# Optimization experiments

Measured on AMD Instinct MI355X. Metric: run time of the kernel, lower is better.

## Reference

```python
import jax, jax.numpy as jnp
import numpy as np

D_MODEL = 1024
D_INNER = 1024
N_HEADS = 16
HEAD_DIM = D_INNER // N_HEADS  # 64
D_STATE = 16
DT_RANK = 16
CHUNK = 64
PROJ = 2 * D_INNER + 2 * D_STATE * N_HEADS + DT_RANK  # 2576


def setup_inputs() -> dict:
    key = jax.random.key(0)
    ks = jax.random.split(key, 6)
    B, S = 4, 4096
    x = jax.random.normal(ks[0], (B, S, D_MODEL), jnp.float32)
    W_in = jax.random.normal(ks[1], (PROJ, D_MODEL), jnp.float32) * 0.02
    dt_W = jax.random.normal(ks[2], (N_HEADS, DT_RANK), jnp.float32) * 0.1
    dt_b = jax.random.normal(ks[3], (N_HEADS,), jnp.float32) * 0.1
    A_log = jnp.full((N_HEADS,), jnp.log(0.5), jnp.float32)
    D_param = jnp.ones((N_HEADS,), jnp.float32)
    W_out = jax.random.normal(ks[4], (D_MODEL, D_INNER), jnp.float32) * 0.02
    norm_w = jnp.ones((D_INNER,), jnp.float32)
    return dict(x=x, W_in=W_in, dt_W=dt_W, dt_b=dt_b, A_log=A_log,
                D_param=D_param, W_out=W_out, norm_w=norm_w)


def _forward(x, W_in, dt_W, dt_b, A_log, D_param, W_out, norm_w):
    B, S, _ = x.shape
    H, P, N, K = N_HEADS, HEAD_DIM, D_STATE, CHUNK
    proj = x @ W_in.T  # (B,S,PROJ)
    xp = proj[..., :D_INNER]
    z = proj[..., D_INNER:2 * D_INNER]
    o = 2 * D_INNER
    B_ssm = proj[..., o:o + N * H].reshape(B, S, H, N)
    C_ssm = proj[..., o + N * H:o + 2 * N * H].reshape(B, S, H, N)
    dt_low = proj[..., o + 2 * N * H:]
    dt = jax.nn.softplus(dt_low @ dt_W.T + dt_b)  # (B,S,H)
    xp = xp.reshape(B, S, H, P)
    A = -jnp.exp(A_log)  # (H,)

    # --- chunked selective scan (SSD) ---
    nC = S // K  # S chosen divisible by K (original pads otherwise)
    xc = xp.reshape(B, nC, K, H, P)
    dtc = dt.reshape(B, nC, K, H)
    Bc = B_ssm.reshape(B, nC, K, H, N)
    Cc = C_ssm.reshape(B, nC, K, H, N)
    dA = dtc * A  # (B,nC,K,H)
    dAcs = jnp.cumsum(dA, axis=2)
    # intra-chunk quadratic (attention-like) form
    Lm = jnp.exp(dAcs[:, :, :, None, :] - dAcs[:, :, None, :, :])
    causal = jnp.tril(jnp.ones((K, K), jnp.float32))
    Lm = Lm * causal[None, None, :, :, None]
    scores = jnp.einsum('bcihn,bcjhn->bcijh', Cc, Bc) * Lm * dtc[:, :, None, :, :]
    y_intra = jnp.einsum('bcijh,bcjhp->bcihp', scores, xc)
    # per-chunk state contribution
    decay_to_end = jnp.exp(dAcs[:, :, -1:, :] - dAcs)
    wx = (dtc * decay_to_end)[..., None] * xc  # (B,nC,K,H,P)
    chunk_state = jnp.einsum('bckhn,bckhp->bchnp', Bc, wx)  # (B,nC,H,N,P)
    chunk_decay = jnp.exp(dAcs[:, :, -1, :])  # (B,nC,H)

    # cross-chunk recurrence: emit state at chunk START (matches torch loop)
    def step(h, inp):
        d, s = inp
        return d[:, :, None, None] * h + s, h
    h0 = jnp.zeros((B, H, N, P), jnp.float32)
    _, h_states = jax.lax.scan(
        step, h0,
        (jnp.moveaxis(chunk_decay, 1, 0), jnp.moveaxis(chunk_state, 1, 0)))
    h_states = jnp.moveaxis(h_states, 0, 1)  # (B,nC,H,N,P)

    y_cross = jnp.einsum('bcthn,bchnp,bcth->bcthp', Cc, h_states, jnp.exp(dAcs))
    y = (y_intra + y_cross).reshape(B, S, H, P)
    # --- end scan ---

    y = y + xp * D_param[None, None, :, None]
    y = y.reshape(B, S, D_INNER)
    rms = jnp.sqrt(jnp.mean(y * y, axis=-1, keepdims=True) + 1e-6)
    y = y / rms * norm_w
    y = y * jax.nn.silu(z)
    return y @ W_out.T


def reference(x, W_in, dt_W, dt_b, A_log, D_param, W_out, norm_w):
    return _forward(x, W_in, dt_W, dt_b, A_log, D_param, W_out, norm_w)
```

## Files before the change

### kernel.cpp

```cpp
#include <hip/hip_runtime.h>

typedef unsigned short u16;
typedef __attribute__((ext_vector_type(8))) short short8;
typedef __attribute__((ext_vector_type(4))) float f32x4;
typedef __attribute__((ext_vector_type(4))) unsigned short u16x4;
typedef __attribute__((ext_vector_type(8))) unsigned short u16x8;

#define BTOK 16384
#define PROJ_N 2576
#define PROJ_PAD 2816
#define DK 1024
#define NCH 256
#define NH 16
#define HD 64
#define NS 16

__device__ __forceinline__ float b2f(u16 b) {
    union { unsigned int u; float f; } v; v.u = ((unsigned int)b) << 16; return v.f;
}
__device__ __forceinline__ u16 f2b(float f) {
    union { float f; unsigned int u; } v; v.f = f;
    unsigned int r = v.u + 0x7fffu + ((v.u >> 16) & 1u);
    return (u16)(r >> 16);
}

__device__ __forceinline__ void stage_asm(const u16* g, const u16* l) {
    unsigned loff = (unsigned)(size_t)(const __attribute__((address_space(3))) u16*)l;
    unsigned su = __builtin_amdgcn_readfirstlane(loff);
    asm volatile("s_mov_b32 m0, %1\n\t"
                 "global_load_lds_dwordx4 %0, off"
                 :: "v"(g), "s"(su));
}

template <int IMM>
__device__ __forceinline__ short8 dsr128(unsigned a) {
    short8 d;
    asm volatile("ds_read_b128 %0, %1 offset:%2" : "=v"(d) : "v"(a), "i"(IMM));
    return d;
}

#define LGKM(n) do { asm volatile("s_waitcnt lgkmcnt(" #n ")"); __builtin_amdgcn_sched_barrier(0); } while (0)
#define MFMA_B16 __builtin_amdgcn_mfma_f32_16x16x32_bf16

__global__ __launch_bounds__(256) void cast_bf16(const float* __restrict__ s,
                                                 u16* __restrict__ d, int n4) {
    int t = blockIdx.x * 256 + threadIdx.x;
    if (t < n4) {
        float4 v = ((const float4*)s)[t];
        u16x4 o; o.x = f2b(v.x); o.y = f2b(v.y); o.z = f2b(v.z); o.w = f2b(v.w);
        ((u16x4*)d)[t] = o;
    }
}

__global__ __launch_bounds__(256) void cast_pad_win(const float* __restrict__ s,
                                                    u16* __restrict__ d) {
    int t = blockIdx.x * 256 + threadIdx.x;
    int i4 = t * 4;
    float4 v = make_float4(0.f, 0.f, 0.f, 0.f);
    if (i4 < PROJ_N * DK) v = ((const float4*)s)[t];
    u16x4 o; o.x = f2b(v.x); o.y = f2b(v.y); o.z = f2b(v.z); o.w = f2b(v.w);
    ((u16x4*)d)[t] = o;
}

#define MT 64

template <int OUT_BF16>
__global__ __launch_bounds__(512, 2) void gemm8(const u16* __restrict__ A,
                                                const u16* __restrict__ B,
                                                float* __restrict__ Cf,
                                                u16* __restrict__ Cb,
                                                int K, int ldc) {
    extern __shared__ u16 smem[];
    u16* AsU = smem;
    const int tid = threadIdx.x;
    const int wave = tid >> 6, lane = tid & 63;
    const int wr = wave >> 2, wc = wave & 3;
    const int m_l = lane & 15, quad = lane >> 4;

    const int b = blockIdx.x;
    const int bm = (b & 7) * 8 + ((b >> 3) & 7);
    const int bn = b >> 6;

    const u16* Ab = A + (long)bm * 256 * K;
    const u16* Bb = B + (long)bn * 256 * K;

    const unsigned lds0 = (unsigned)(size_t)(const __attribute__((address_space(3))) u16*)smem;
    const int sw = m_l & 7;
    const unsigned a0b = lds0 + (wr * 128 + m_l) * 128 + (quad ^ sw) * 16;
    const unsigned a1b = lds0 + (wr * 128 + m_l) * 128 + ((4 + quad) ^ sw) * 16;
    const unsigned b0b = lds0 + 65536 + (wc * 64 + m_l) * 128 + (quad ^ sw) * 16;
    const unsigned b1b = lds0 + 65536 + (wc * 64 + m_l) * 128 + ((4 + quad) ^ sw) * 16;

    const int srow = tid >> 3;
    const int schk = (tid & 7) ^ (srow & 7);
    const int sdst = wave * 512;

    f32x4 acc[8][4];
#pragma unroll
    for (int f = 0; f < 8; ++f)
#pragma unroll
        for (int n = 0; n < 4; ++n) acc[f][n] = (f32x4){0.f, 0.f, 0.f, 0.f};

    const int NT = K >> 6;

    auto stage = [&](const u16* G, u16* L, int q, int k0) {
        stage_asm(G + (long)(q * 64 + srow) * K + k0 + schk * 8,
                  L + q * 4096 + sdst);
    };
    u16* BsU = smem + 32768;

    stage(Ab, AsU, 0, 0); stage(Ab, AsU, 2, 0);
    stage(Bb, BsU, 0, 0); stage(Bb, BsU, 1, 0); stage(Bb, BsU, 2, 0); stage(Bb, BsU, 3, 0);
    stage(Ab, AsU, 1, 0); stage(Ab, AsU, 3, 0);
    stage(Ab, AsU + 16384, 0, 64); stage(Ab, AsU + 16384, 2, 64);
    asm volatile("s_waitcnt vmcnt(2)");
    __builtin_amdgcn_s_barrier();

    short8 af[4][2], bf[4][2];
    af[0][0] = dsr128<0>(a0b);    af[0][1] = dsr128<0>(a1b);
    af[1][0] = dsr128<2048>(a0b); af[1][1] = dsr128<2048>(a1b);
    af[2][0] = dsr128<4096>(a0b); af[2][1] = dsr128<4096>(a1b);
    af[3][0] = dsr128<6144>(a0b); af[3][1] = dsr128<6144>(a1b);
    bf[0][0] = dsr128<0>(b0b);    bf[0][1] = dsr128<0>(b1b);
    bf[1][0] = dsr128<2048>(b0b); bf[1][1] = dsr128<2048>(b1b);

    int cur = 0;
    for (int t = 0; t < NT; ++t) {
        const unsigned cB = ((unsigned)cur) << 15;
        const unsigned a0 = a0b + cB, a1 = a1b + cB, b0 = b0b + cB, b1 = b1b + cB;
        const int cbu = cur << 14;
        u16* Anxt = AsU + (cbu ^ 16384);
        u16* Bnxt = BsU + (cbu ^ 16384);
        u16* Acur = AsU + cbu;
        const int k1 = (t + 1) << 6, k2 = (t + 2) << 6;
        const bool s1 = (t + 1 < NT), s2 = (t + 2 < NT);

        bf[2][0] = dsr128<4096>(b0); bf[2][1] = dsr128<4096>(b1);
        bf[3][0] = dsr128<6144>(b0); bf[3][1] = dsr128<6144>(b1);
        if (s1) { stage(Bb, Bnxt, 0, k1); stage(Bb, Bnxt, 1, k1);
                  stage(Bb, Bnxt, 2, k1); stage(Bb, Bnxt, 3, k1); }
        __builtin_amdgcn_s_barrier();
        LGKM(4);
        __builtin_amdgcn_s_setprio(1);
#pragma unroll
        for (int f = 0; f < 4; ++f)
#pragma unroll
            for (int n = 0; n < 2; ++n) {
                acc[f][n] = MFMA_B16(af[f][0], bf[n][0], acc[f][n], 0, 0, 0);
                acc[f][n] = MFMA_B16(af[f][1], bf[n][1], acc[f][n], 0, 0, 0);
            }
        __builtin_amdgcn_s_setprio(0);
        __builtin_amdgcn_sched_barrier(0);

        LGKM(0);
        __builtin_amdgcn_s_setprio(1);
#pragma unroll
        for (int f = 0; f < 4; ++f)
#pragma unroll
            for (int n = 0; n < 2; ++n) {
                acc[f][2 + n] = MFMA_B16(af[f][0], bf[2 + n][0], acc[f][2 + n], 0, 0, 0);
                acc[f][2 + n] = MFMA_B16(af[f][1], bf[2 + n][1], acc[f][2 + n], 0, 0, 0);
            }
        __builtin_amdgcn_s_setprio(0);
        __builtin_amdgcn_sched_barrier(0);
        if (s1) { stage(Ab, Anxt, 1, k1); stage(Ab, Anxt, 3, k1); }
        if (s1) { asm volatile("s_waitcnt vmcnt(8)"); }
        else    { asm volatile("s_waitcnt vmcnt(0)"); }
        __builtin_amdgcn_s_barrier();

        af[0][0] = dsr128<8192>(a0);  af[0][1] = dsr128<8192>(a1);
        af[1][0] = dsr128<10240>(a0); af[1][1] = dsr128<10240>(a1);
        af[2][0] = dsr128<12288>(a0); af[2][1] = dsr128<12288>(a1);
        af[3][0] = dsr128<14336>(a0); af[3][1] = dsr128<14336>(a1);
        if (s2) { stage(Ab, Acur, 0, k2); stage(Ab, Acur, 2, k2); }
        __builtin_amdgcn_s_setprio(1);
        LGKM(6);
#pragma unroll
        for (int n = 0; n < 2; ++n) {
            acc[4][n] = MFMA_B16(af[0][0], bf[n][0], acc[4][n], 0, 0, 0);
            acc[4][n] = MFMA_B16(af[0][1], bf[n][1], acc[4][n], 0, 0, 0);
        }
        LGKM(4);
#pragma unroll
        for (int n = 0; n < 2; ++n) {
            acc[5][n] = MFMA_B16(af[1][0], bf[n][0], acc[5][n], 0, 0, 0);
            acc[5][n] = MFMA_B16(af[1][1], bf[n][1], acc[5][n], 0, 0, 0);
        }
        LGKM(2);
#pragma unroll
        for (int n = 0; n < 2; ++n) {
            acc[6][n] = MFMA_B16(af[2][0], bf[n][0], acc[6][n], 0, 0, 0);
            acc[6][n] = MFMA_B16(af[2][1], bf[n][1], acc[6][n], 0, 0, 0);
        }
        LGKM(0);
#pragma unroll
        for (int n = 0; n < 2; ++n) {
            acc[7][n] = MFMA_B16(af[3][0], bf[n][0], acc[7][n], 0, 0, 0);
            acc[7][n] = MFMA_B16(af[3][1], bf[n][1], acc[7][n], 0, 0, 0);
        }
#pragma unroll
        for (int f = 0; f < 4; ++f)
#pragma unroll
            for (int n = 0; n < 2; ++n) {
                acc[4 + f][2 + n] = MFMA_B16(af[f][0], bf[2 + n][0], acc[4 + f][2 + n], 0, 0, 0);
                acc[4 + f][2 + n] = MFMA_B16(af[f][1], bf[2 + n][1], acc[4 + f][2 + n], 0, 0, 0);
            }
        __builtin_amdgcn_s_setprio(0);
        __builtin_amdgcn_sched_barrier(0);

        if (s1 && s2)      { asm volatile("s_waitcnt vmcnt(4)"); }
        else if (s1)       { asm volatile("s_waitcnt vmcnt(2)"); }
        __builtin_amdgcn_s_barrier();
        if (s1) {
            const unsigned nB = cB ^ 32768u;
            const unsigned na0 = a0b + nB, na1 = a1b + nB, nb0 = b0b + nB, nb1 = b1b + nB;
            af[0][0] = dsr128<0>(na0);    af[0][1] = dsr128<0>(na1);
            af[1][0] = dsr128<2048>(na0); af[1][1] = dsr128<2048>(na1);
            af[2][0] = dsr128<4096>(na0); af[2][1] = dsr128<4096>(na1);
            af[3][0] = dsr128<6144>(na0); af[3][1] = dsr128<6144>(na1);
            bf[0][0] = dsr128<0>(nb0);    bf[0][1] = dsr128<0>(nb1);
            bf[1][0] = dsr128<2048>(nb0); bf[1][1] = dsr128<2048>(nb1);
        }
        cur ^= 1;
    }

#pragma unroll
    for (int f = 0; f < 8; ++f) {
        int row_base = bm * 256 + wr * 128 + f * 16 + quad * 4;
#pragma unroll
        for (int n = 0; n < 4; ++n) {
            int col = bn * 256 + wc * 64 + n * 16 + m_l;
#pragma unroll
            for (int r = 0; r < 4; ++r) {
                float v = acc[f][n][r];
                long off = (long)(row_base + r) * ldc + col;
                if (OUT_BF16) Cb[off] = f2b(v);
                else          Cf[off] = v;
            }
        }
    }
}

__global__ __launch_bounds__(256) void ssm_intra(const u16* __restrict__ proj,
                                                 const float* __restrict__ dt_W,
                                                 const float* __restrict__ dt_b,
                                                 const float* __restrict__ A_log,
                                                 float* __restrict__ dAcs,
                                                 float* __restrict__ decay,
                                                 u16* __restrict__ y_acc,
                                                 float* __restrict__ cstate) {
    int bch = blockIdx.x;
    int bc = bch >> 4, h = bch & 15;
    long tok0 = (long)bc * 64;
    __shared__ float Cs[64][20], Bm[64][20];
    __shared__ u16 Sh[64][72], Sl[64][72];
    __shared__ u16 Xt[64][72];
    __shared__ u16 Wh[64][72], Wl[64][72];
    __shared__ u16 Bt[16][72];
    __shared__ float dts[64], dAs[64], wk[64];
    const int tid = threadIdx.x;
    const int wave = tid >> 6, lane = tid & 63;
    const int m_l = lane & 15, quad = lane >> 4;

    if (tid < 64) {
        long tok = tok0 + tid;
        u16x8 lo0 = *(const u16x8*)&proj[tok * PROJ_PAD + 2560];
        u16x8 lo1 = *(const u16x8*)&proj[tok * PROJ_PAD + 2568];
        float a = dt_b[h];
#pragma unroll
        for (int r = 0; r < 8; ++r) a += b2f(lo0[r]) * dt_W[h * 16 + r];
#pragma unroll
        for (int r = 0; r < 8; ++r) a += b2f(lo1[r]) * dt_W[h * 16 + 8 + r];
        float d = (a > 20.f) ? a : log1pf(__expf(a));
        float dA = -__expf(A_log[h]) * d;
        float cs = dA;
#pragma unroll
        for (int off = 1; off < 64; off <<= 1) {
            float o = __shfl_up(cs, off, 64);
            if (tid >= off) cs += o;
        }
        float cs63 = __shfl(cs, 63, 64);
        dts[tid] = d;
        dAs[tid] = cs;
        wk[tid] = d * __expf(cs63 - cs);
        dAcs[tok * 16 + h] = cs;
        if (tid == 63) decay[bc * 16 + h] = __expf(cs);
    }
#pragma unroll
    for (int it = 0; it < 4; ++it) {
        int li = it * 256 + tid;
        int i = li >> 4, n = li & 15;
        u16 cb = proj[(tok0 + i) * PROJ_PAD + 2304 + h * 16 + n];
        u16 bb = proj[(tok0 + i) * PROJ_PAD + 2048 + h * 16 + n];
        Cs[i][n] = b2f(cb);
        Bm[i][n] = b2f(bb);
        Bt[n][i] = bb;
    }
    __syncthreads();
#pragma unroll
    for (int it = 0; it < 2; ++it) {
        int li = it * 256 + tid;
        int j = li & 63, p0 = (li >> 6) * 8;
        u16x8 xv = *(const u16x8*)&proj[(tok0 + j) * PROJ_PAD + h * 64 + p0];
        float w = wk[j];
#pragma unroll
        for (int t = 0; t < 8; ++t) {
            u16 xb = xv[t];
            Xt[p0 + t][j] = xb;
            float v = w * b2f(xb);
            u16 hi = f2b(v);
            Wh[p0 + t][j] = hi;
            Wl[p0 + t][j] = f2b(v - b2f(hi));
        }
    }
    {
        int j = tid & 63, i0 = tid >> 6;
#pragma unroll
        for (int g = 0; g < 16; ++g) {
            int i = i0 + g * 4;
            float v = 0.f;
            if (j <= i) {
                float d = 0.f;
                const f32x4* cp = (const f32x4*)Cs[i];
                const f32x4* bp = (const f32x4*)Bm[j];
#pragma unroll
                for (int n4 = 0; n4 < 4; ++n4) {
                    f32x4 c = cp[n4], b = bp[n4];
                    d += c.x * b.x + c.y * b.y + c.z * b.z + c.w * b.w;
                }
                v = d * __expf(dAs[i] - dAs[j]) * dts[j];
            }
            u16 hi = f2b(v);
            Sh[i][j] = hi;
            Sl[i][j] = f2b(v - b2f(hi));
        }
    }
    __syncthreads();
    {
        f32x4 yv[4];
#pragma unroll
        for (int jt = 0; jt < 4; ++jt) yv[jt] = (f32x4){0.f, 0.f, 0.f, 0.f};
#pragma unroll
        for (int ks = 0; ks < 2; ++ks) {
            int kc = ks * 32 + quad * 8;
            short8 ah = *(const short8*)&Sh[wave * 16 + m_l][kc];
            short8 al = *(const short8*)&Sl[wave * 16 + m_l][kc];
#pragma unroll
            for (int jt = 0; jt < 4; ++jt) {
                short8 bx = *(const short8*)&Xt[jt * 16 + m_l][kc];
                yv[jt] = MFMA_B16(ah, bx, yv[jt], 0, 0, 0);
                yv[jt] = MFMA_B16(al, bx, yv[jt], 0, 0, 0);
            }
        }
#pragma unroll
        for (int jt = 0; jt < 4; ++jt)
#pragma unroll
            for (int r = 0; r < 4; ++r) {
                int i = wave * 16 + quad * 4 + r;
                int p = jt * 16 + m_l;
                y_acc[(tok0 + i) * 1024 + h * 64 + p] = f2b(yv[jt][r]);
            }
    }
    {
        f32x4 cacc = (f32x4){0.f, 0.f, 0.f, 0.f};
#pragma unroll
        for (int ks = 0; ks < 2; ++ks) {
            int kc = ks * 32 + quad * 8;
            short8 a = *(const short8*)&Bt[m_l][kc];
            short8 bh = *(const short8*)&Wh[wave * 16 + m_l][kc];
            short8 bl = *(const short8*)&Wl[wave * 16 + m_l][kc];
            cacc = MFMA_B16(a, bh, cacc, 0, 0, 0);
            cacc = MFMA_B16(a, bl, cacc, 0, 0, 0);
        }
#pragma unroll
        for (int r = 0; r < 4; ++r) {
            int n = quad * 4 + r;
            int p = wave * 16 + m_l;
            cstate[(long)bch * 1024 + n * 64 + p] = cacc[r];
        }
    }
}

__global__ __launch_bounds__(256) void scan_chunks(const float* __restrict__ cs,
                                                   const float* __restrict__ decay,
                                                   float* __restrict__ hs) {
    int t = blockIdx.x * 256 + threadIdx.x;
    int p = t & 63, n = (t >> 6) & 15, h = (t >> 10) & 15, b = t >> 14;
    float state = 0.f;
    for (int c = 0; c < 64; ++c) {
        long idx = (((long)((b * 64 + c) * 16 + h)) * 16 + n) * 64 + p;
        hs[idx] = state;
        state = decay[(b * 64 + c) * 16 + h] * state + cs[idx];
    }
}

__global__ __launch_bounds__(256) void ssm_cross(const u16* __restrict__ proj,
                                                 const float* __restrict__ dAcs,
                                                 const float* __restrict__ hs,
                                                 const u16* __restrict__ y_acc,
                                                 const float* __restrict__ D_param,
                                                 u16* __restrict__ y_pre) {
    int bch = blockIdx.x;
    int bc = bch >> 4, h = bch & 15;
    long tok0 = (long)bc * 64;
    __shared__ float hss[16][64], Cs[64][16], dAs[64];
    int tid = threadIdx.x;
#pragma unroll
    for (int it = 0; it < 4; ++it) {
        int li = it * 256 + tid;
        hss[li >> 6][li & 63] = hs[(long)bch * 1024 + li];
        int i = li >> 4, n = li & 15;
        Cs[i][n] = b2f(proj[(tok0 + i) * PROJ_PAD + 2304 + h * 16 + n]);
    }
    if (tid < 64) dAs[tid] = dAcs[(tok0 + tid) * 16 + h];
    __syncthreads();
    float Dh = D_param[h];
    int pi = (tid & 15) * 4;
    int ib = tid >> 4;
#pragma unroll
    for (int g = 0; g < 4; ++g) {
        int i = ib + 16 * g;
        f32x4 cr = (f32x4){0.f, 0.f, 0.f, 0.f};
#pragma unroll
        for (int n = 0; n < 16; ++n) {
            float c = Cs[i][n];
            cr += c * *(const f32x4*)&hss[n][pi];
        }
        float e = __expf(dAs[i]);
        long off = (tok0 + i) * 1024 + h * 64 + pi;
        u16x4 ya = *(const u16x4*)&y_acc[off];
        u16x4 xv = *(const u16x4*)&proj[(tok0 + i) * PROJ_PAD + h * 64 + pi];
        u16x4 o;
        o.x = f2b(b2f(ya.x) + e * cr.x + b2f(xv.x) * Dh);
        o.y = f2b(b2f(ya.y) + e * cr.y + b2f(xv.y) * Dh);
        o.z = f2b(b2f(ya.z) + e * cr.z + b2f(xv.z) * Dh);
        o.w = f2b(b2f(ya.w) + e * cr.w + b2f(xv.w) * Dh);
        *(u16x4*)&y_pre[off] = o;
    }
}

__global__ __launch_bounds__(256) void norm_gate(const u16* __restrict__ proj,
                                                 const float* __restrict__ norm_w,
                                                 u16* __restrict__ y) {
    long tok = blockIdx.x;
    int tid = threadIdx.x;
    int c0 = tid * 4;
    u16x4 yv = *(const u16x4*)&y[tok * 1024 + c0];
    float v0 = b2f(yv.x), v1 = b2f(yv.y), v2 = b2f(yv.z), v3 = b2f(yv.w);
    float ss = v0 * v0 + v1 * v1 + v2 * v2 + v3 * v3;
    int lane = tid & 63, w = tid >> 6;
#pragma unroll
    for (int d = 32; d > 0; d >>= 1) ss += __shfl_down(ss, d, 64);
    __shared__ float red[4];
    if (lane == 0) red[w] = ss;
    __syncthreads();
    float tot = red[0] + red[1] + red[2] + red[3];
    float inv = rsqrtf(tot * (1.f / 1024.f) + 1e-6f);
    float4 nw = *(const float4*)&norm_w[c0];
    u16x4 zv = *(const u16x4*)&proj[tok * PROJ_PAD + 1024 + c0];
    float z0 = b2f(zv.x), z1 = b2f(zv.y), z2 = b2f(zv.z), z3 = b2f(zv.w);
    u16x4 o;
    o.x = f2b(v0 * inv * nw.x * (z0 / (1.f + __expf(-z0))));
    o.y = f2b(v1 * inv * nw.y * (z1 / (1.f + __expf(-z1))));
    o.z = f2b(v2 * inv * nw.z * (z2 / (1.f + __expf(-z2))));
    o.w = f2b(v3 * inv * nw.w * (z3 / (1.f + __expf(-z3))));
    *(u16x4*)&y[tok * 1024 + c0] = o;
}

extern "C" void kernel_launch(void* const* d_in, const int* in_sizes, int n_in,
                              void* d_out, int out_size, void* d_ws, size_t ws_size,
                              hipStream_t stream) {
    const float* x      = (const float*)d_in[0];
    const float* W_in   = (const float*)d_in[1];
    const float* dt_W   = (const float*)d_in[2];
    const float* dt_b   = (const float*)d_in[3];
    const float* A_log  = (const float*)d_in[4];
    const float* D_par  = (const float*)d_in[5];
    const float* W_out  = (const float*)d_in[6];
    const float* norm_w = (const float*)d_in[7];
    float* out = (float*)d_out;

    char* ws = (char*)d_ws;
    size_t off = 0;
    auto alloc = [&](size_t b) { void* p = ws + off; off += (b + 255) & ~(size_t)255; return p; };
    u16*   x_bf    = (u16*)alloc((size_t)BTOK * DK * 2);
    u16*   win_bf  = (u16*)alloc((size_t)PROJ_PAD * DK * 2);
    u16*   wout_bf = (u16*)alloc((size_t)DK * DK * 2);
    u16*   proj    = (u16*)alloc((size_t)BTOK * PROJ_PAD * 2);
    float* dAcs    = (float*)alloc((size_t)BTOK * NH * 4);
    float* decay   = (float*)alloc((size_t)NCH * NH * 4);
    float* cstate  = (float*)alloc((size_t)NCH * NH * NS * HD * 4);
    float* hstates = (float*)alloc((size_t)NCH * NH * NS * HD * 4);
    u16*   y_pre   = (u16*)alloc((size_t)BTOK * DK * 2);
    u16*   y_acc   = x_bf;

    static bool attr_done = false;
    if (!attr_done) {
        (void)hipFuncSetAttribute(reinterpret_cast<const void*>(&gemm8<1>),
                                  hipFuncAttributeMaxDynamicSharedMemorySize, 131072);
        (void)hipFuncSetAttribute(reinterpret_cast<const void*>(&gemm8<0>),
                                  hipFuncAttributeMaxDynamicSharedMemorySize, 131072);
        attr_done = true;
    }

    cast_bf16<<<BTOK * DK / 4 / 256, 256, 0, stream>>>(x, x_bf, BTOK * DK / 4);
    cast_bf16<<<DK * DK / 4 / 256, 256, 0, stream>>>(W_out, wout_bf, DK * DK / 4);
    cast_pad_win<<<PROJ_PAD * DK / 4 / 256, 256, 0, stream>>>(W_in, win_bf);

    gemm8<1><<<dim3(MT * (PROJ_PAD / 256)), 512, 131072, stream>>>(x_bf, win_bf, nullptr, proj, DK, PROJ_PAD);

    ssm_intra<<<NCH * NH, 256, 0, stream>>>(proj, dt_W, dt_b, A_log, dAcs, decay, y_acc, cstate);
    scan_chunks<<<256, 256, 0, stream>>>(cstate, decay, hstates);
    ssm_cross<<<NCH * NH, 256, 0, stream>>>(proj, dAcs, hstates, y_acc, D_par, y_pre);
    norm_gate<<<BTOK, 256, 0, stream>>>(proj, norm_w, y_pre);

    gemm8<0><<<dim3(MT * (DK / 256)), 512, 131072, stream>>>(y_pre, wout_bf, out, nullptr, DK, DK);
}
```

Before: 389.5 us.

## Restructure GEMM main loop into four k-split phases with single barrier per tile

Rewrites the bf16 MFMA GEMM inner loop so each 64-wide k tile is processed in four phases over k-halves and row halves. Global stages for the next tile are interleaved with LDS fragment reads and MFMA blocks, and there is one vmcnt(0) wait plus one barrier per iteration instead of several partial waits and barriers. The intent is to cut synchronisation overhead and make LDS reads and MFMAs overlap better. The trade-off is a shallower prefetch: only one tile ahead instead of partly two, and the full vmcnt(0) wait may expose global-memory latency.

Measured after the change: 379.0 us. 1.03x faster.

```diff
diff --git a/kernel.cpp b/kernel.cpp
--- a/kernel.cpp
+++ b/kernel.cpp
@@ -65,7 +65,7 @@
 #define MT 64
 
 template <int OUT_BF16>
-__global__ __launch_bounds__(512, 2) void gemm8(const u16* __restrict__ A,
+__global__ __launch_bounds__(512, 2) void gemmk(const u16* __restrict__ A,
                                                 const u16* __restrict__ B,
                                                 float* __restrict__ Cf,
                                                 u16* __restrict__ Cb,
@@ -109,117 +109,85 @@
     };
     u16* BsU = smem + 32768;
 
-    stage(Ab, AsU, 0, 0); stage(Ab, AsU, 2, 0);
+    stage(Ab, AsU, 0, 0); stage(Ab, AsU, 1, 0); stage(Ab, AsU, 2, 0); stage(Ab, AsU, 3, 0);
     stage(Bb, BsU, 0, 0); stage(Bb, BsU, 1, 0); stage(Bb, BsU, 2, 0); stage(Bb, BsU, 3, 0);
-    stage(Ab, AsU, 1, 0); stage(Ab, AsU, 3, 0);
-    stage(Ab, AsU + 16384, 0, 64); stage(Ab, AsU + 16384, 2, 64);
-    asm volatile("s_waitcnt vmcnt(2)");
+    asm volatile("s_waitcnt vmcnt(0)");
     __builtin_amdgcn_s_barrier();
 
-    short8 af[4][2], bf[4][2];
-    af[0][0] = dsr128<0>(a0b);    af[0][1] = dsr128<0>(a1b);
-    af[1][0] = dsr128<2048>(a0b); af[1][1] = dsr128<2048>(a1b);
-    af[2][0] = dsr128<4096>(a0b); af[2][1] = dsr128<4096>(a1b);
-    af[3][0] = dsr128<6144>(a0b); af[3][1] = dsr128<6144>(a1b);
-    bf[0][0] = dsr128<0>(b0b);    bf[0][1] = dsr128<0>(b1b);
-    bf[1][0] = dsr128<2048>(b0b); bf[1][1] = dsr128<2048>(b1b);
+    short8 afX[4], afY[4], bfX[4], bfY[4];
+    afX[0] = dsr128<0>(a0b);    afX[1] = dsr128<2048>(a0b);
+    afX[2] = dsr128<4096>(a0b); afX[3] = dsr128<6144>(a0b);
+    bfX[0] = dsr128<0>(b0b);    bfX[1] = dsr128<2048>(b0b);
+    bfX[2] = dsr128<4096>(b0b); bfX[3] = dsr128<6144>(b0b);
 
     int cur = 0;
     for (int t = 0; t < NT; ++t) {
         const unsigned cB = ((unsigned)cur) << 15;
         const unsigned a0 = a0b + cB, a1 = a1b + cB, b0 = b0b + cB, b1 = b1b + cB;
-        const int cbu = cur << 14;
-        u16* Anxt = AsU + (cbu ^ 16384);
-        u16* Bnxt = BsU + (cbu ^ 16384);
-        u16* Acur = AsU + cbu;
-        const int k1 = (t + 1) << 6, k2 = (t + 2) << 6;
-        const bool s1 = (t + 1 < NT), s2 = (t + 2 < NT);
-
-        bf[2][0] = dsr128<4096>(b0); bf[2][1] = dsr128<4096>(b1);
-        bf[3][0] = dsr128<6144>(b0); bf[3][1] = dsr128<6144>(b1);
-        if (s1) { stage(Bb, Bnxt, 0, k1); stage(Bb, Bnxt, 1, k1);
-                  stage(Bb, Bnxt, 2, k1); stage(Bb, Bnxt, 3, k1); }
-        __builtin_amdgcn_s_barrier();
+        const int nbu = (cur << 14) ^ 16384;
+        u16* Anxt = AsU + nbu;
+        u16* Bnxt = BsU + nbu;
+        const int k1 = (t + 1) << 6;
+        const bool s1 = (t + 1 < NT);
+
+        if (s1) { stage(Ab, Anxt, 0, k1); stage(Ab, Anxt, 1, k1); }
+        afY[0] = dsr128<8192>(a0);  afY[1] = dsr128<10240>(a0);
+        afY[2] = dsr128<12288>(a0); afY[3] = dsr128<14336>(a0);
         LGKM(4);
         __builtin_amdgcn_s_setprio(1);
 #pragma unroll
         for (int f = 0; f < 4; ++f)
 #pragma unroll
-            for (int n = 0; n < 2; ++n) {
-                acc[f][n] = MFMA_B16(af[f][0], bf[n][0], acc[f][n], 0, 0, 0);
-                acc[f][n] = MFMA_B16(af[f][1], bf[n][1], acc[f][n], 0, 0, 0);
-            }
+            for (int n = 0; n < 4; ++n)
+                acc[f][n] = MFMA_B16(afX[f], bfX[n], acc[f][n], 0, 0, 0);
+        __builtin_amdgcn_s_setprio(0);
+
+        if (s1) { stage(Ab, Anxt, 2, k1); stage(Ab, Anxt, 3, k1); }
+        afX[0] = dsr128<0>(a1);    afX[1] = dsr128<2048>(a1);
+        afX[2] = dsr128<4096>(a1); afX[3] = dsr128<6144>(a1);
+        bfY[0] = dsr128<0>(b1);    bfY[1] = dsr128<2048>(b1);
+        bfY[2] = dsr128<4096>(b1); bfY[3] = dsr128<6144>(b1);
+        LGKM(8);
+        __builtin_amdgcn_s_setprio(1);
+#pragma unroll
+        for (int f = 0; f < 4; ++f)
+#pragma unroll
+            for (int n = 0; n < 4; ++n)
+                acc[4 + f][n] = MFMA_B16(afY[f], bfX[n], acc[4 + f][n], 0, 0, 0);
+        __builtin_amdgcn_s_setprio(0);
+
+        if (s1) { stage(Bb, Bnxt, 0, k1); stage(Bb, Bnxt, 1, k1); }
+        afY[0] = dsr128<8192>(a1);  afY[1] = dsr128<10240>(a1);
+        afY[2] = dsr128<12288>(a1); afY[3] = dsr128<14336>(a1);
+        LGKM(4);
+        __builtin_amdgcn_s_setprio(1);
+#pragma unroll
+        for (int f = 0; f < 4; ++f)
+#pragma unroll
+            for (int n = 0; n < 4; ++n)
+                acc[f][n] = MFMA_B16(afX[f], bfY[n], acc[f][n], 0, 0, 0);
+        __builtin_amdgcn_s_setprio(0);
+
+        if (s1) { stage(Bb, Bnxt, 2, k1); stage(Bb, Bnxt, 3, k1); }
+        LGKM(0);
+        __builtin_amdgcn_s_setprio(1);
+#pragma unroll
+        for (int f = 0; f < 4; ++f)
+#pragma unroll
+            for (int n = 0; n < 4; ++n)
+                acc[4 + f][n] = MFMA_B16(afY[f], bfY[n], acc[4 + f][n], 0, 0, 0);
         __builtin_amdgcn_s_setprio(0);
         __builtin_amdgcn_sched_barrier(0);
 
-        LGKM(0);
-        __builtin_amdgcn_s_setprio(1);
-#pragma unroll
-        for (int f = 0; f < 4; ++f)
-#pragma unroll
-            for (int n = 0; n < 2; ++n) {
-                acc[f][2 + n] = MFMA_B16(af[f][0], bf[2 + n][0], acc[f][2 + n], 0, 0, 0);
-                acc[f][2 + n] = MFMA_B16(af[f][1], bf[2 + n][1], acc[f][2 + n], 0, 0, 0);
-            }
-        __builtin_amdgcn_s_setprio(0);
-        __builtin_amdgcn_sched_barrier(0);
-        if (s1) { stage(Ab, Anxt, 1, k1); stage(Ab, Anxt, 3, k1); }
-        if (s1) { asm volatile("s_waitcnt vmcnt(8)"); }
-        else    { asm volatile("s_waitcnt vmcnt(0)"); }
-        __builtin_amdgcn_s_barrier();
-
-        af[0][0] = dsr128<8192>(a0);  af[0][1] = dsr128<8192>(a1);
-        af[1][0] = dsr128<10240>(a0); af[1][1] = dsr128<10240>(a1);
-        af[2][0] = dsr128<12288>(a0); af[2][1] = dsr128<12288>(a1);
-        af[3][0] = dsr128<14336>(a0); af[3][1] = dsr128<14336>(a1);
-        if (s2) { stage(Ab, Acur, 0, k2); stage(Ab, Acur, 2, k2); }
-        __builtin_amdgcn_s_setprio(1);
-        LGKM(6);
-#pragma unroll
-        for (int n = 0; n < 2; ++n) {
-            acc[4][n] = MFMA_B16(af[0][0], bf[n][0], acc[4][n], 0, 0, 0);
-            acc[4][n] = MFMA_B16(af[0][1], bf[n][1], acc[4][n], 0, 0, 0);
-        }
-        LGKM(4);
-#pragma unroll
-        for (int n = 0; n < 2; ++n) {
-            acc[5][n] = MFMA_B16(af[1][0], bf[n][0], acc[5][n], 0, 0, 0);
-            acc[5][n] = MFMA_B16(af[1][1], bf[n][1], acc[5][n], 0, 0, 0);
-        }
-        LGKM(2);
-#pragma unroll
-        for (int n = 0; n < 2; ++n) {
-            acc[6][n] = MFMA_B16(af[2][0], bf[n][0], acc[6][n], 0, 0, 0);
-            acc[6][n] = MFMA_B16(af[2][1], bf[n][1], acc[6][n], 0, 0, 0);
-        }
-        LGKM(0);
-#pragma unroll
-        for (int n = 0; n < 2; ++n) {
-            acc[7][n] = MFMA_B16(af[3][0], bf[n][0], acc[7][n], 0, 0, 0);
-            acc[7][n] = MFMA_B16(af[3][1], bf[n][1], acc[7][n], 0, 0, 0);
-        }
-#pragma unroll
-        for (int f = 0; f < 4; ++f)
-#pragma unroll
-            for (int n = 0; n < 2; ++n) {
-                acc[4 + f][2 + n] = MFMA_B16(af[f][0], bf[2 + n][0], acc[4 + f][2 + n], 0, 0, 0);
-                acc[4 + f][2 + n] = MFMA_B16(af[f][1], bf[2 + n][1], acc[4 + f][2 + n], 0, 0, 0);
-            }
-        __builtin_amdgcn_s_setprio(0);
-        __builtin_amdgcn_sched_barrier(0);
-
-        if (s1 && s2)      { asm volatile("s_waitcnt vmcnt(4)"); }
-        else if (s1)       { asm volatile("s_waitcnt vmcnt(2)"); }
-        __builtin_amdgcn_s_barrier();
         if (s1) {
+            asm volatile("s_waitcnt vmcnt(0)");
+            __builtin_amdgcn_s_barrier();
             const unsigned nB = cB ^ 32768u;
-            const unsigned na0 = a0b + nB, na1 = a1b + nB, nb0 = b0b + nB, nb1 = b1b + nB;
-            af[0][0] = dsr128<0>(na0);    af[0][1] = dsr128<0>(na1);
-            af[1][0] = dsr128<2048>(na0); af[1][1] = dsr128<2048>(na1);
-            af[2][0] = dsr128<4096>(na0); af[2][1] = dsr128<4096>(na1);
-            af[3][0] = dsr128<6144>(na0); af[3][1] = dsr128<6144>(na1);
-            bf[0][0] = dsr128<0>(nb0);    bf[0][1] = dsr128<0>(nb1);
-            bf[1][0] = dsr128<2048>(nb0); bf[1][1] = dsr128<2048>(nb1);
+            const unsigned na0 = a0b + nB, nb0 = b0b + nB;
+            afX[0] = dsr128<0>(na0);    afX[1] = dsr128<2048>(na0);
+            afX[2] = dsr128<4096>(na0); afX[3] = dsr128<6144>(na0);
+            bfX[0] = dsr128<0>(nb0);    bfX[1] = dsr128<2048>(nb0);
+            bfX[2] = dsr128<4096>(nb0); bfX[3] = dsr128<6144>(nb0);
         }
         cur ^= 1;
     }
@@ -496,9 +464,9 @@
 
     static bool attr_done = false;
     if (!attr_done) {
-        (void)hipFuncSetAttribute(reinterpret_cast<const void*>(&gemm8<1>),
+        (void)hipFuncSetAttribute(reinterpret_cast<const void*>(&gemmk<1>),
                                   hipFuncAttributeMaxDynamicSharedMemorySize, 131072);
-        (void)hipFuncSetAttribute(reinterpret_cast<const void*>(&gemm8<0>),
+        (void)hipFuncSetAttribute(reinterpret_cast<const void*>(&gemmk<0>),
                                   hipFuncAttributeMaxDynamicSharedMemorySize, 131072);
         attr_done = true;
     }
@@ -507,12 +475,12 @@
     cast_bf16<<<DK * DK / 4 / 256, 256, 0, stream>>>(W_out, wout_bf, DK * DK / 4);
     cast_pad_win<<<PROJ_PAD * DK / 4 / 256, 256, 0, stream>>>(W_in, win_bf);
 
-    gemm8<1><<<dim3(MT * (PROJ_PAD / 256)), 512, 131072, stream>>>(x_bf, win_bf, nullptr, proj, DK, PROJ_PAD);
+    gemmk<1><<<dim3(MT * (PROJ_PAD / 256)), 512, 131072, stream>>>(x_bf, win_bf, nullptr, proj, DK, PROJ_PAD);
 
     ssm_intra<<<NCH * NH, 256, 0, stream>>>(proj, dt_W, dt_b, A_log, dAcs, decay, y_acc, cstate);
     scan_chunks<<<256, 256, 0, stream>>>(cstate, decay, hstates);
     ssm_cross<<<NCH * NH, 256, 0, stream>>>(proj, dAcs, hstates, y_acc, D_par, y_pre);
     norm_gate<<<BTOK, 256, 0, stream>>>(proj, norm_w, y_pre);
 
-    gemm8<0><<<dim3(MT * (DK / 256)), 512, 131072, stream>>>(y_pre, wout_bf, out, nullptr, DK, DK);
-}
+    gemmk<0><<<dim3(MT * (DK / 256)), 512, 131072, stream>>>(y_pre, wout_bf, out, nullptr, DK, DK);
+}
```
